# Kernel tuning notes

Measured on AMD Instinct MI355X. Metric: run time of the kernel, lower is better.

## Reference

```python
import math
import jax, jax.numpy as jnp
import numpy as np

B, T, E = 2, 2048, 1024
H, KV = 16, 4
D = E // H          # 64
G = H // KV         # 4 groups


def rotate_half(x):
    x1, x2 = jnp.split(x, 2, axis=-1)
    return jnp.concatenate([-x2, x1], axis=-1)


def setup_inputs() -> dict:
    key = jax.random.key(0)
    ks = jax.random.split(key, 12)
    query = jax.random.normal(ks[0], (B, T, E), jnp.float32)
    key_t = jax.random.normal(ks[1], (B, T, E), jnp.float32)
    value = jax.random.normal(ks[2], (B, T, E), jnp.float32)
    # RoPE tables: [T, D]
    inv_freq = 1.0 / (10000.0 ** (np.arange(0, D, 2, dtype=np.float32) / D))
    pos = np.arange(T, dtype=np.float32)
    freqs = np.outer(pos, inv_freq)                      # [T, D/2]
    emb = np.concatenate([freqs, freqs], axis=-1)        # [T, D]
    cos_emb = jnp.asarray(np.cos(emb), jnp.float32)
    sin_emb = jnp.asarray(np.sin(emb), jnp.float32)
    # causal mask [1,1,T,T], True = keep
    mask = jnp.tril(jnp.ones((T, T), bool))[None, None, :, :]
    s = 0.02
    Wq = jax.random.normal(ks[3], (E, H * D), jnp.float32) * s
    bq = jnp.zeros((H * D,), jnp.float32)
    Wk = jax.random.normal(ks[4], (E, KV * D), jnp.float32) * s
    bk = jnp.zeros((KV * D,), jnp.float32)
    Wv = jax.random.normal(ks[5], (E, KV * D), jnp.float32) * s
    bv = jnp.zeros((KV * D,), jnp.float32)
    Wo = jax.random.normal(ks[6], (E, E), jnp.float32) * s
    bo = jnp.zeros((E,), jnp.float32)
    return {"query": query, "key": key_t, "value": value,
            "cos_emb": cos_emb, "sin_emb": sin_emb, "mask": mask,
            "Wq": Wq, "bq": bq, "Wk": Wk, "bk": bk,
            "Wv": Wv, "bv": bv, "Wo": Wo, "bo": bo}


def reference(query, key, value, cos_emb, sin_emb, mask,
              Wq, bq, Wk, bk, Wv, bv, Wo, bo):
    Bq, Tq, _ = query.shape
    Tk = key.shape[1]
    q = (query @ Wq + bq).reshape(Bq, Tq, H, D)          # [B,Tq,H,D]
    k = (key @ Wk + bk).reshape(Bq, Tk, KV, D)           # [B,Tk,KV,D]
    v = (value @ Wv + bv).reshape(Bq, Tk, KV, D)
    # expand kv heads across groups (head h = kv*G + g, consecutive repeat)
    k = jnp.repeat(k, G, axis=2)                         # [B,Tk,H,D]
    v = jnp.repeat(v, G, axis=2)
    # RoPE (applied post-expansion, as in the original)
    cos = cos_emb[None, :, None, :]                      # [1,T,1,D]
    sin = sin_emb[None, :, None, :]
    q = q * cos[:, :Tq] + rotate_half(q) * sin[:, :Tq]
    k = k * cos[:, :Tk] + rotate_half(k) * sin[:, :Tk]
    scores = jnp.einsum('bqhd,bkhd->bhqk', q, k) / math.sqrt(D)
    scores = jnp.where(mask[:, :, :Tq, :Tk], scores, jnp.float32(-jnp.inf))
    probs = jax.nn.softmax(scores, axis=-1)              # [B,H,Tq,Tk]
    attn = jnp.einsum('bhqk,bkhd->bqhd', probs, v).reshape(Bq, Tq, E)
    return attn @ Wo + bo
```

## Files before the change

kernel.cpp:

```cpp
#include <hip/hip_runtime.h>
#include <hip/hip_bf16.h>

constexpr int Bc  = 2;
constexpr int Tc  = 2048;
constexpr int Ec  = 1024;
constexpr int Hc  = 16;
constexpr int KVc = 4;
constexpr int Dc  = 64;

typedef short bf16x8 __attribute__((ext_vector_type(8)));
typedef short short4v __attribute__((ext_vector_type(4)));
typedef float f32x4  __attribute__((ext_vector_type(4)));
typedef float f32x16 __attribute__((ext_vector_type(16)));
typedef int   i32x4  __attribute__((ext_vector_type(4)));

__device__ inline short f2bf_bits(float f) {
    union { __hip_bfloat16 h; short s; } u;
    u.h = __float2bfloat16(f);
    return u.s;
}

__device__ inline float bf2f(short s) {
    union { short s16; __hip_bfloat16 h; } u;
    u.s16 = s;
    return __bfloat162float(u.h);
}

__device__ inline unsigned pkbf(float a, float b) {
    union { __hip_bfloat162 h2; unsigned u; } u;
    u.h2 = __float22bfloat162_rn(float2{a, b});
    return u.u;
}

__device__ inline float fexp2(float x) { return __builtin_exp2f(x); }

__device__ inline void permswap(unsigned &a, unsigned &b) {
    asm volatile("v_permlane32_swap_b32 %0, %1" : "+v"(a), "+v"(b));
}

__device__ inline void gload16(const short* g, short* lds) {
    __builtin_amdgcn_global_load_lds(
        (const __attribute__((address_space(1))) unsigned int*)g,
        (__attribute__((address_space(3))) unsigned int*)lds,
        16, 0, 0);
}

__global__ __launch_bounds__(256) void transp_all(
    const float* __restrict__ Wq, const float* __restrict__ Wk,
    const float* __restrict__ Wv, const float* __restrict__ Wo,
    short* __restrict__ Wqt, short* __restrict__ Wkt,
    short* __restrict__ Wvt, short* __restrict__ Wot)
{
    __shared__ float tile[32][33];
    const int id = blockIdx.x;
    const float* W; short* Wt; int N, bx, by;
    if (id < 1024)      { W = Wq; Wt = Wqt; N = 1024; bx = id & 31;          by = id >> 5; }
    else if (id < 1280) { W = Wk; Wt = Wkt; N = 256;  bx = (id - 1024) & 7;  by = (id - 1024) >> 3; }
    else if (id < 1536) { W = Wv; Wt = Wvt; N = 256;  bx = (id - 1280) & 7;  by = (id - 1280) >> 3; }
    else                { W = Wo; Wt = Wot; N = 1024; bx = (id - 1536) & 31; by = (id - 1536) >> 5; }
    const int K = 1024;
    int nb = bx * 32, kb = by * 32;
    int tx = threadIdx.x & 31, ty = threadIdx.x >> 5;
    #pragma unroll
    for (int j = 0; j < 4; ++j)
        tile[ty + j * 8][tx] = W[(size_t)(kb + ty + j * 8) * N + nb + tx];
    __syncthreads();
    #pragma unroll
    for (int j = 0; j < 4; ++j)
        Wt[(size_t)(nb + ty + j * 8) * K + kb + tx] = f2bf_bits(tile[tx][ty + j * 8]);
}

__global__ __launch_bounds__(256) void gemm_qkv(
    const float* __restrict__ Xq, const float* __restrict__ Xk,
    const float* __restrict__ Xv,
    const short* __restrict__ Wqt, const short* __restrict__ Wkt,
    const short* __restrict__ Wvt,
    const float* __restrict__ bq, const float* __restrict__ bk,
    const float* __restrict__ bv,
    short* __restrict__ Qp, short* __restrict__ Kp, short* __restrict__ VTp)
{
    __shared__ short As[128 * 64];
    __shared__ short Bs[64 * 64];
    const int gid = blockIdx.x;
    const float* A; const short* Bt; const float* bias; int bx, by, mode;
    if (gid < 512)      { mode = 0; A = Xq; Bt = Wqt; bias = bq; bx = gid & 15;         by = gid >> 4; }
    else if (gid < 640) { mode = 1; A = Xk; Bt = Wkt; bias = bk; bx = (gid - 512) & 3;  by = (gid - 512) >> 2; }
    else                { mode = 2; A = Xv; Bt = Wvt; bias = bv; bx = (gid - 640) & 3;  by = (gid - 640) >> 2; }
    const int m0 = by * 128, n0 = bx * 64;

    const int lane = threadIdx.x & 63;
    const int w    = threadIdx.x >> 6;
    const int wm   = w >> 1, wn = w & 1;
    const int rin  = lane >> 3;
    const int swc  = ((lane & 7) ^ rin) * 8;

    f32x4 acc[4][2] = {};

    for (int k0 = 0; k0 < 1024; k0 += 64) {
        #pragma unroll
        for (int it = 0; it < 4; ++it) {
            int s   = threadIdx.x + it * 256;
            int row = s >> 3;
            int c8  = s & 7;
            const float* src = A + (size_t)(m0 + row) * 1024 + k0 + c8 * 8;
            float4 f0 = *reinterpret_cast<const float4*>(src);
            float4 f1 = *reinterpret_cast<const float4*>(src + 4);
            union { unsigned u4[4]; bf16x8 v; } pk;
            pk.u4[0] = pkbf(f0.x, f0.y);
            pk.u4[1] = pkbf(f0.z, f0.w);
            pk.u4[2] = pkbf(f1.x, f1.y);
            pk.u4[3] = pkbf(f1.z, f1.w);
            *reinterpret_cast<bf16x8*>(As + row * 64 + ((c8 ^ (row & 7)) * 8)) = pk.v;
        }
        #pragma unroll
        for (int i2 = 0; i2 < 2; ++i2) {
            const int r = w * 16 + i2 * 8;
            gload16(Bt + (size_t)(n0 + r + rin) * 1024 + k0 + swc, Bs + r * 64);
        }
        __syncthreads();
        #pragma unroll
        for (int ks = 0; ks < 2; ++ks) {
            bf16x8 af[4], bfr[2];
            #pragma unroll
            for (int mi = 0; mi < 4; ++mi) {
                int row = wm * 64 + mi * 16 + (lane & 15);
                int sl  = (ks * 4 + (lane >> 4)) ^ (row & 7);
                af[mi] = *reinterpret_cast<const bf16x8*>(As + row * 64 + sl * 8);
            }
            #pragma unroll
            for (int ni = 0; ni < 2; ++ni) {
                int row = wn * 32 + ni * 16 + (lane & 15);
                int sl  = (ks * 4 + (lane >> 4)) ^ (row & 7);
                bfr[ni] = *reinterpret_cast<const bf16x8*>(Bs + row * 64 + sl * 8);
            }
            #pragma unroll
            for (int mi = 0; mi < 4; ++mi)
                #pragma unroll
                for (int ni = 0; ni < 2; ++ni)
                    acc[mi][ni] = __builtin_amdgcn_mfma_f32_16x16x32_bf16(
                        af[mi], bfr[ni], acc[mi][ni], 0, 0, 0);
        }
        __syncthreads();
    }

    #pragma unroll
    for (int mi = 0; mi < 4; ++mi)
        #pragma unroll
        for (int ni = 0; ni < 2; ++ni) {
            int col = n0 + wn * 32 + ni * 16 + (lane & 15);
            float bv2 = bias[col];
            #pragma unroll
            for (int i = 0; i < 4; ++i) {
                int row = m0 + wm * 64 + mi * 16 + ((lane >> 4) * 4) + i;
                float v = acc[mi][ni][i] + bv2;
                if (mode == 0)
                    Qp[(size_t)row * 1024 + col] = f2bf_bits(v);
                else if (mode == 1)
                    Kp[(size_t)row * 256 + col] = f2bf_bits(v);
                else
                    VTp[(((size_t)(row >> 11) * 256 + col) << 11) + (row & 2047)]
                        = f2bf_bits(v);
            }
        }
}

__global__ __launch_bounds__(256) void gemm_o(
    const short* __restrict__ A, const short* __restrict__ Bt,
    const float* __restrict__ bias, float* __restrict__ C)
{
    __shared__ short As[128 * 64];
    __shared__ short Bs[64 * 64];
    const int m0 = blockIdx.y * 128, n0 = blockIdx.x * 64;

    const int lane = threadIdx.x & 63;
    const int w    = threadIdx.x >> 6;
    const int wm   = w >> 1, wn = w & 1;
    const int rin  = lane >> 3;
    const int swc  = ((lane & 7) ^ rin) * 8;

    f32x4 acc[4][2] = {};

    for (int k0 = 0; k0 < 1024; k0 += 64) {
        #pragma unroll
        for (int i2 = 0; i2 < 4; ++i2) {
            const int r = w * 32 + i2 * 8;
            gload16(A + (size_t)(m0 + r + rin) * 1024 + k0 + swc, As + r * 64);
        }
        #pragma unroll
        for (int i2 = 0; i2 < 2; ++i2) {
            const int r = w * 16 + i2 * 8;
            gload16(Bt + (size_t)(n0 + r + rin) * 1024 + k0 + swc, Bs + r * 64);
        }
        __syncthreads();
        #pragma unroll
        for (int ks = 0; ks < 2; ++ks) {
            bf16x8 af[4], bfr[2];
            #pragma unroll
            for (int mi = 0; mi < 4; ++mi) {
                int row = wm * 64 + mi * 16 + (lane & 15);
                int sl  = (ks * 4 + (lane >> 4)) ^ (row & 7);
                af[mi] = *reinterpret_cast<const bf16x8*>(As + row * 64 + sl * 8);
            }
            #pragma unroll
            for (int ni = 0; ni < 2; ++ni) {
                int row = wn * 32 + ni * 16 + (lane & 15);
                int sl  = (ks * 4 + (lane >> 4)) ^ (row & 7);
                bfr[ni] = *reinterpret_cast<const bf16x8*>(Bs + row * 64 + sl * 8);
            }
            #pragma unroll
            for (int mi = 0; mi < 4; ++mi)
                #pragma unroll
                for (int ni = 0; ni < 2; ++ni)
                    acc[mi][ni] = __builtin_amdgcn_mfma_f32_16x16x32_bf16(
                        af[mi], bfr[ni], acc[mi][ni], 0, 0, 0);
        }
        __syncthreads();
    }

    #pragma unroll
    for (int mi = 0; mi < 4; ++mi)
        #pragma unroll
        for (int ni = 0; ni < 2; ++ni) {
            int col = n0 + wn * 32 + ni * 16 + (lane & 15);
            float bv2 = bias[col];
            #pragma unroll
            for (int i = 0; i < 4; ++i) {
                int row = m0 + wm * 64 + mi * 16 + ((lane >> 4) * 4) + i;
                C[(size_t)row * 1024 + col] = acc[mi][ni][i] + bv2;
            }
        }
}

__global__ __launch_bounds__(256) void rope_k(
    short* __restrict__ Kp,
    const float* __restrict__ cosE, const float* __restrict__ sinE)
{
    int idx = blockIdx.x * 256 + threadIdx.x;
    int dq  = (idx & 7) * 4;
    int hh  = (idx >> 3) & 3;
    int row = idx >> 5;
    int t   = row & (Tc - 1);
    float4 c4 = *reinterpret_cast<const float4*>(cosE + t * 64 + dq);
    float4 s4 = *reinterpret_cast<const float4*>(sinE + t * 64 + dq);
    size_t base = (size_t)row * 256 + hh * 64 + dq;
    short4v a = *reinterpret_cast<const short4v*>(Kp + base);
    short4v b = *reinterpret_cast<const short4v*>(Kp + base + 32);
    short4v oa, ob;
    float c[4] = {c4.x, c4.y, c4.z, c4.w};
    float s[4] = {s4.x, s4.y, s4.z, s4.w};
    #pragma unroll
    for (int j = 0; j < 4; ++j) {
        float x1 = bf2f(a[j]), x2 = bf2f(b[j]);
        oa[j] = f2bf_bits(x1 * c[j] - x2 * s[j]);
        ob[j] = f2bf_bits(x2 * c[j] + x1 * s[j]);
    }
    *reinterpret_cast<short4v*>(Kp + base)      = oa;
    *reinterpret_cast<short4v*>(Kp + base + 32) = ob;
}

__global__ __launch_bounds__(256, 3) void flash_gqa9(
    const short* __restrict__ Q,
    const short* __restrict__ Kx,
    const short* __restrict__ VT,
    const float* __restrict__ cosE,
    const float* __restrict__ sinE,
    short* __restrict__ attn,
    short* __restrict__ PO,
    float* __restrict__ ML)
{
    __shared__ short smem[16384];

    const int lane = threadIdx.x & 63;
    const int w    = threadIdx.x >> 6;
    const int lo   = lane & 31;
    const int hi   = lane >> 5;

    const int L   = blockIdx.x;
    const int xcd = L & 7;
    const int j   = L >> 3;
    const int g   = j & 3;
    const int u   = 39 - (j >> 2);
    int qt = 0, rem = u;
    while (true) { int nc0 = (qt >> 2) + 1; if (rem < nc0) break; rem -= nc0; ++qt; }
    const int c  = rem;
    const int nc = (qt >> 2) + 1;
    const int b   = xcd >> 2;
    const int kvh = xcd & 3;
    const int h   = kvh * 4 + g;
    const int slot = (b * 16 + h) * 40 + u;

    const int q0w = qt * 128 + w * 32;
    const int qg  = q0w + lo;

    bf16x8 qf[4];
    {
        const short* qp = Q + (size_t)(b * Tc + qg) * Ec + h * 64 + hi * 8;
        const float* ct = cosE + (size_t)qg * 64 + hi * 8;
        const float* st = sinE + (size_t)qg * 64 + hi * 8;
        float qv[4][8], cv[4][8], sv[4][8];
        #pragma unroll
        for (int ds = 0; ds < 4; ++ds) {
            bf16x8 raw = *reinterpret_cast<const bf16x8*>(qp + 16 * ds);
            float4 c0 = *reinterpret_cast<const float4*>(ct + 16 * ds);
            float4 c1 = *reinterpret_cast<const float4*>(ct + 16 * ds + 4);
            float4 s0 = *reinterpret_cast<const float4*>(st + 16 * ds);
            float4 s1 = *reinterpret_cast<const float4*>(st + 16 * ds + 4);
            #pragma unroll
            for (int j2 = 0; j2 < 8; ++j2) qv[ds][j2] = bf2f(raw[j2]);
            cv[ds][0] = c0.x; cv[ds][1] = c0.y; cv[ds][2] = c0.z; cv[ds][3] = c0.w;
            cv[ds][4] = c1.x; cv[ds][5] = c1.y; cv[ds][6] = c1.z; cv[ds][7] = c1.w;
            sv[ds][0] = s0.x; sv[ds][1] = s0.y; sv[ds][2] = s0.z; sv[ds][3] = s0.w;
            sv[ds][4] = s1.x; sv[ds][5] = s1.y; sv[ds][6] = s1.z; sv[ds][7] = s1.w;
        }
        constexpr float SC = 0.125f * 1.44269504089f;
        #pragma unroll
        for (int ds = 0; ds < 2; ++ds) {
            #pragma unroll
            for (int j2 = 0; j2 < 8; j2 += 2) {
                float a0 = (qv[ds][j2]     * cv[ds][j2]     - qv[ds+2][j2]     * sv[ds][j2])     * SC;
                float a1 = (qv[ds][j2+1]   * cv[ds][j2+1]   - qv[ds+2][j2+1]   * sv[ds][j2+1])   * SC;
                float b0 = (qv[ds+2][j2]   * cv[ds+2][j2]   + qv[ds][j2]       * sv[ds+2][j2])   * SC;
                float b1 = (qv[ds+2][j2+1] * cv[ds+2][j2+1] + qv[ds][j2+1]     * sv[ds+2][j2+1]) * SC;
                reinterpret_cast<unsigned*>(&qf[ds])[j2 >> 1]     = pkbf(a0, a1);
                reinterpret_cast<unsigned*>(&qf[ds + 2])[j2 >> 1] = pkbf(b0, b1);
            }
        }
    }
    const short* Kb = Kx + (size_t)b * Tc * (KVc * Dc) + kvh * 64;
    const short* Vb = VT + (size_t)(b * KVc + kvh) * 64 * Tc;

    const int rin = lane >> 3;
    const int swc = ((lane & 7) ^ rin) * 8;
    auto stage = [&](int bufi, int kb2) {
        #pragma unroll
        for (int i2 = 0; i2 < 2; ++i2) {
            const int row = w * 16 + i2 * 8;
            gload16(Kb + (size_t)(kb2 + row + rin) * 256 + swc,
                    smem + bufi * 4096 + row * 64);
            gload16(Vb + (size_t)(row + rin) * Tc + kb2 + swc,
                    smem + 8192 + bufi * 4096 + row * 64);
        }
    };

    int slot8[4];
    #pragma unroll
    for (int i = 0; i < 4; ++i)
        slot8[i] = (((2 * i + hi) ^ (lo & 7)) * 8) + lo * 64;

    const int t0 = c * 8;
    const int t1 = min(c * 8 + 8, 2 * qt + 2);
    stage(0, t0 * 64);

    float m = -1e30f, l = 0.f;
    f32x16 o0 = {}, o1 = {};
    const int kv_hi = q0w + 32;

    for (int t = t0; t < t1; ++t) {
        const int kb  = t * 64;
        const int cur = (t - t0) & 1;
        asm volatile("s_waitcnt vmcnt(0)" ::: "memory");
        __builtin_amdgcn_s_barrier();
        if (t + 1 < t1) stage(cur ^ 1, kb + 64);

        if (kb < kv_hi) {
            const short* Kl = smem + cur * 4096;
            const short* Vl = Kl + 8192;

            bf16x8 kf0[4], kf1[4];
            #pragma unroll
            for (int ds = 0; ds < 4; ++ds) {
                kf0[ds] = *reinterpret_cast<const bf16x8*>(Kl + slot8[ds]);
                kf1[ds] = *reinterpret_cast<const bf16x8*>(Kl + slot8[ds] + 2048);
            }

            f32x16 s0 = {}, s1 = {};
            __builtin_amdgcn_s_setprio(1);
            #pragma unroll
            for (int ds = 0; ds < 4; ++ds) {
                s0 = __builtin_amdgcn_mfma_f32_32x32x16_bf16(kf0[ds], qf[ds], s0, 0, 0, 0);
                s1 = __builtin_amdgcn_mfma_f32_32x32x16_bf16(kf1[ds], qf[ds], s1, 0, 0, 0);
            }
            __builtin_amdgcn_s_setprio(0);

            bf16x8 vf0[4], vf1[4];
            #pragma unroll
            for (int sl = 0; sl < 4; ++sl) {
                vf0[sl] = *reinterpret_cast<const bf16x8*>(Vl + slot8[sl]);
                vf1[sl] = *reinterpret_cast<const bf16x8*>(Vl + slot8[sl] + 2048);
            }

            if (kb + 63 > q0w) {
                #pragma unroll
                for (int r = 0; r < 16; ++r) {
                    int kkl = (r & 3) + 8 * (r >> 2) + 4 * hi;
                    if (kb + kkl > qg)      s0[r] = -1e30f;
                    if (kb + 32 + kkl > qg) s1[r] = -1e30f;
                }
            }

            float mx[8];
            #pragma unroll
            for (int j2 = 0; j2 < 8; ++j2)
                mx[j2] = fmaxf(fmaxf(s0[2 * j2], s0[2 * j2 + 1]),
                               fmaxf(s1[2 * j2], s1[2 * j2 + 1]));
            #pragma unroll
            for (int st = 4; st > 0; st >>= 1)
                #pragma unroll
                for (int j2 = 0; j2 < st; ++j2) mx[j2] = fmaxf(mx[j2], mx[j2 + st]);
            float pm = fmaxf(mx[0], __shfl_xor(mx[0], 32));

            float corr = 1.0f;
            if (__any(pm > m + 8.0f)) {
                float mn = fmaxf(m, pm);
                corr = fexp2(m - mn);
                m = mn;
                #pragma unroll
                for (int r = 0; r < 16; ++r) { o0[r] *= corr; o1[r] *= corr; }
            }
            float rs = 0.f;
            #pragma unroll
            for (int r = 0; r < 16; ++r) {
                s0[r] = fexp2(s0[r] - m);
                s1[r] = fexp2(s1[r] - m);
                rs += s0[r] + s1[r];
            }
            rs += __shfl_xor(rs, 32);
            l = l * corr + rs;

            #pragma unroll
            for (int t2 = 0; t2 < 2; ++t2) {
                const f32x16& sv2 = t2 ? s1 : s0;
                unsigned pw[8];
                #pragma unroll
                for (int j2 = 0; j2 < 8; ++j2)
                    pw[j2] = pkbf(sv2[2 * j2], sv2[2 * j2 + 1]);
                #pragma unroll
                for (int u2 = 0; u2 < 2; ++u2) {
                    permswap(pw[4 * u2 + 0], pw[4 * u2 + 2]);
                    permswap(pw[4 * u2 + 1], pw[4 * u2 + 3]);
                    union { unsigned u4[4]; bf16x8 v; } pf;
                    pf.u4[0] = pw[4 * u2 + 0];
                    pf.u4[1] = pw[4 * u2 + 1];
                    pf.u4[2] = pw[4 * u2 + 2];
                    pf.u4[3] = pw[4 * u2 + 3];
                    int sl = 2 * t2 + u2;
                    __builtin_amdgcn_s_setprio(1);
                    o0 = __builtin_amdgcn_mfma_f32_32x32x16_bf16(vf0[sl], pf.v, o0, 0, 0, 0);
                    o1 = __builtin_amdgcn_mfma_f32_32x32x16_bf16(vf1[sl], pf.v, o1, 0, 0, 0);
                    __builtin_amdgcn_s_setprio(0);
                }
            }
        }
    }
    __builtin_amdgcn_s_barrier();

    const float inv = (nc == 1) ? (1.0f / l) : 1.0f;
    short* ob = smem + w * 2048;
    #pragma unroll
    for (int r = 0; r < 16; ++r) {
        int d0 = (r & 3) + 8 * (r >> 2) + 4 * hi;
        ob[lo * 64 + ( d0       ^ ((lo & 7) << 3))] = f2bf_bits(o0[r] * inv);
        ob[lo * 64 + ((d0 + 32) ^ ((lo & 7) << 3))] = f2bf_bits(o1[r] * inv);
    }
    if (nc > 1 && hi == 0) {
        ML[(size_t)slot * 256 + (w * 32 + lo) * 2]     = m;
        ML[(size_t)slot * 256 + (w * 32 + lo) * 2 + 1] = l;
    }
    #pragma unroll
    for (int j2 = 0; j2 < 4; ++j2) {
        int row = lane >> 1;
        int c8  = ((lane & 1) * 4 + j2) * 8;
        bf16x8 v = *reinterpret_cast<const bf16x8*>(
            ob + row * 64 + (c8 ^ ((row & 7) << 3)));
        if (nc == 1)
            *reinterpret_cast<bf16x8*>(
                attn + (size_t)(b * Tc + q0w + row) * Ec + h * 64 + c8) = v;
        else
            *reinterpret_cast<bf16x8*>(
                PO + (size_t)slot * 8192 + (w * 32 + row) * 64 + c8) = v;
    }
}

__global__ __launch_bounds__(256) void combine_kernel(
    const short* __restrict__ PO, const float* __restrict__ ML,
    short* __restrict__ attn)
{
    const int qt    = 4 + (blockIdx.x >> 2);
    const int rg    = blockIdx.x & 3;
    const int combo = blockIdx.y;
    const int h = combo & 15, b = combo >> 4;
    const int nc = (qt >> 2) + 1;
    const int k  = qt >> 2, r4 = qt & 3;
    const int base = (k + 1) * (2 * k + r4);
    const int slot0 = combo * 40 + base;

    const int r  = rg * 32 + (threadIdx.x >> 3);
    const int d8 = (threadIdx.x & 7) * 8;

    float mv[4], lv[4];
    float M = -1e30f;
    #pragma unroll 4
    for (int cc = 0; cc < nc; ++cc) {
        mv[cc] = ML[(size_t)(slot0 + cc) * 256 + r * 2];
        lv[cc] = ML[(size_t)(slot0 + cc) * 256 + r * 2 + 1];
        M = fmaxf(M, mv[cc]);
    }
    float Lsum = 0.f;
    float a[8] = {};
    #pragma unroll 4
    for (int cc = 0; cc < nc; ++cc) {
        float wgt = fexp2(mv[cc] - M);
        Lsum += wgt * lv[cc];
        bf16x8 po = *reinterpret_cast<const bf16x8*>(
            PO + (size_t)(slot0 + cc) * 8192 + r * 64 + d8);
        #pragma unroll
        for (int j = 0; j < 8; ++j) a[j] += wgt * bf2f(po[j]);
    }
    float inv = 1.0f / Lsum;
    bf16x8 o;
    #pragma unroll
    for (int j = 0; j < 8; ++j) o[j] = f2bf_bits(a[j] * inv);
    *reinterpret_cast<bf16x8*>(
        attn + (size_t)(b * Tc + qt * 128 + r) * Ec + h * 64 + d8) = o;
}

extern "C" void kernel_launch(void* const* d_in, const int* in_sizes, int n_in,
                              void* d_out, int out_size, void* d_ws, size_t ws_size,
                              hipStream_t stream)
{
    const float* query = (const float*)d_in[0];
    const float* key   = (const float*)d_in[1];
    const float* value = (const float*)d_in[2];
    const float* cosE  = (const float*)d_in[3];
    const float* sinE  = (const float*)d_in[4];
    const float* Wq = (const float*)d_in[6];
    const float* bq = (const float*)d_in[7];
    const float* Wk = (const float*)d_in[8];
    const float* bk = (const float*)d_in[9];
    const float* Wv = (const float*)d_in[10];
    const float* bv = (const float*)d_in[11];
    const float* Wo = (const float*)d_in[12];
    const float* bo = (const float*)d_in[13];

    char* ws = (char*)d_ws;
    constexpr size_t MB = 1u << 20;
    short* PO   = (short*)(ws + 0);
    float* ML   = (float*)(ws + 21 * MB);
    short* Wqt  = (short*)(ws + 24 * MB);
    short* Wkt  = (short*)(ws + 26 * MB);
    short* Wvt  = (short*)(ws + 26 * MB + 512 * 1024);
    short* Wot  = (short*)(ws + 27 * MB);
    short* Qp   = (short*)(ws + 29 * MB);
    short* Kp   = (short*)(ws + 37 * MB);
    short* VTp  = (short*)(ws + 39 * MB);
    short* attn = (short*)(ws + 41 * MB);
    (void)ws_size;

    transp_all<<<2560, 256, 0, stream>>>(Wq, Wk, Wv, Wo, Wqt, Wkt, Wvt, Wot);
    gemm_qkv<<<768, 256, 0, stream>>>(query, key, value, Wqt, Wkt, Wvt,
                                      bq, bk, bv, Qp, Kp, VTp);
    rope_k<<<512, 256, 0, stream>>>(Kp, cosE, sinE);
    flash_gqa9<<<1280, 256, 0, stream>>>(Qp, Kp, VTp, cosE, sinE, attn, PO, ML);
    combine_kernel<<<dim3(48, 32), 256, 0, stream>>>(PO, ML, attn);
    gemm_o<<<dim3(16, 32), 256, 0, stream>>>(attn, Wot, bo, (float*)d_out);
}
```

Measured before the change: 133.4 us.

## Fuse RoPE into QKV GEMM epilogue, pre-convert query to bf16, lighten flash registers

Adds a kernel that converts the query activations to bf16 so the Q-projection GEMM can stream its A tile into shared memory through global_load_lds. Q and K RoPE, together with the softmax scale for Q, now run in the GEMM epilogue via a shared-memory staged tile, which removes the separate rope_k kernel and the per-block Q RoPE in the flash kernel. The flash kernel loads K and V fragments just before each MFMA rather than holding them all in registers, and its launch bound rises from 3 to 4 waves per SIMD to raise occupancy. In exchange it adds an extra pass over the query input and one more kernel launch.

```diff
diff --git a/kernel.cpp b/kernel.cpp
--- a/kernel.cpp
+++ b/kernel.cpp
@@ -43,6 +43,19 @@
         (const __attribute__((address_space(1))) unsigned int*)g,
         (__attribute__((address_space(3))) unsigned int*)lds,
         16, 0, 0);
+}
+
+__global__ __launch_bounds__(256) void conv_q(
+    const float* __restrict__ q, short* __restrict__ Xq)
+{
+    int i = (blockIdx.x * 256 + threadIdx.x) * 4;
+    float4 vv = *reinterpret_cast<const float4*>(q + i);
+    short4v o;
+    o[0] = f2bf_bits(vv.x);
+    o[1] = f2bf_bits(vv.y);
+    o[2] = f2bf_bits(vv.z);
+    o[3] = f2bf_bits(vv.w);
+    *reinterpret_cast<short4v*>(Xq + i) = o;
 }
 
 __global__ __launch_bounds__(256) void transp_all(
@@ -71,21 +84,23 @@
 }
 
 __global__ __launch_bounds__(256) void gemm_qkv(
-    const float* __restrict__ Xq, const float* __restrict__ Xk,
-    const float* __restrict__ Xv,
+    const short* __restrict__ Xq,
+    const float* __restrict__ keyF, const float* __restrict__ valF,
     const short* __restrict__ Wqt, const short* __restrict__ Wkt,
     const short* __restrict__ Wvt,
     const float* __restrict__ bq, const float* __restrict__ bk,
     const float* __restrict__ bv,
+    const float* __restrict__ cosE, const float* __restrict__ sinE,
     short* __restrict__ Qp, short* __restrict__ Kp, short* __restrict__ VTp)
 {
     __shared__ short As[128 * 64];
     __shared__ short Bs[64 * 64];
     const int gid = blockIdx.x;
-    const float* A; const short* Bt; const float* bias; int bx, by, mode;
-    if (gid < 512)      { mode = 0; A = Xq; Bt = Wqt; bias = bq; bx = gid & 15;         by = gid >> 4; }
-    else if (gid < 640) { mode = 1; A = Xk; Bt = Wkt; bias = bk; bx = (gid - 512) & 3;  by = (gid - 512) >> 2; }
-    else                { mode = 2; A = Xv; Bt = Wvt; bias = bv; bx = (gid - 640) & 3;  by = (gid - 640) >> 2; }
+    const short* Bt; const float* bias; int bx, by, mode;
+    const float* Af = nullptr;
+    if (gid < 512)      { mode = 0; Bt = Wqt; bias = bq; bx = gid & 15;        by = gid >> 4; }
+    else if (gid < 640) { mode = 1; Af = keyF; Bt = Wkt; bias = bk; bx = (gid - 512) & 3; by = (gid - 512) >> 2; }
+    else                { mode = 2; Af = valF; Bt = Wvt; bias = bv; bx = (gid - 640) & 3; by = (gid - 640) >> 2; }
     const int m0 = by * 128, n0 = bx * 64;
 
     const int lane = threadIdx.x & 63;
@@ -97,20 +112,28 @@
     f32x4 acc[4][2] = {};
 
     for (int k0 = 0; k0 < 1024; k0 += 64) {
-        #pragma unroll
-        for (int it = 0; it < 4; ++it) {
-            int s   = threadIdx.x + it * 256;
-            int row = s >> 3;
-            int c8  = s & 7;
-            const float* src = A + (size_t)(m0 + row) * 1024 + k0 + c8 * 8;
-            float4 f0 = *reinterpret_cast<const float4*>(src);
-            float4 f1 = *reinterpret_cast<const float4*>(src + 4);
-            union { unsigned u4[4]; bf16x8 v; } pk;
-            pk.u4[0] = pkbf(f0.x, f0.y);
-            pk.u4[1] = pkbf(f0.z, f0.w);
-            pk.u4[2] = pkbf(f1.x, f1.y);
-            pk.u4[3] = pkbf(f1.z, f1.w);
-            *reinterpret_cast<bf16x8*>(As + row * 64 + ((c8 ^ (row & 7)) * 8)) = pk.v;
+        if (mode == 0) {
+            #pragma unroll
+            for (int i2 = 0; i2 < 4; ++i2) {
+                const int r = w * 32 + i2 * 8;
+                gload16(Xq + (size_t)(m0 + r + rin) * 1024 + k0 + swc, As + r * 64);
+            }
+        } else {
+            #pragma unroll
+            for (int it = 0; it < 4; ++it) {
+                int s   = threadIdx.x + it * 256;
+                int row = s >> 3;
+                int c8  = s & 7;
+                const float* src = Af + (size_t)(m0 + row) * 1024 + k0 + c8 * 8;
+                float4 f0 = *reinterpret_cast<const float4*>(src);
+                float4 f1 = *reinterpret_cast<const float4*>(src + 4);
+                union { unsigned u4[4]; bf16x8 v; } pk;
+                pk.u4[0] = pkbf(f0.x, f0.y);
+                pk.u4[1] = pkbf(f0.z, f0.w);
+                pk.u4[2] = pkbf(f1.x, f1.y);
+                pk.u4[3] = pkbf(f1.z, f1.w);
+                *reinterpret_cast<bf16x8*>(As + row * 64 + ((c8 ^ (row & 7)) * 8)) = pk.v;
+            }
         }
         #pragma unroll
         for (int i2 = 0; i2 < 2; ++i2) {
@@ -143,25 +166,63 @@
         __syncthreads();
     }
 
+    if (mode == 2) {
+        #pragma unroll
+        for (int mi = 0; mi < 4; ++mi)
+            #pragma unroll
+            for (int ni = 0; ni < 2; ++ni) {
+                int col = n0 + wn * 32 + ni * 16 + (lane & 15);
+                float bv2 = bias[col];
+                #pragma unroll
+                for (int i = 0; i < 4; ++i) {
+                    int row = m0 + wm * 64 + mi * 16 + ((lane >> 4) * 4) + i;
+                    VTp[(((size_t)(row >> 11) * 256 + col) << 11) + (row & 2047)]
+                        = f2bf_bits(acc[mi][ni][i] + bv2);
+                }
+            }
+        return;
+    }
+
     #pragma unroll
     for (int mi = 0; mi < 4; ++mi)
         #pragma unroll
         for (int ni = 0; ni < 2; ++ni) {
-            int col = n0 + wn * 32 + ni * 16 + (lane & 15);
-            float bv2 = bias[col];
+            int cl = wn * 32 + ni * 16 + (lane & 15);
+            float bv2 = bias[n0 + cl];
             #pragma unroll
             for (int i = 0; i < 4; ++i) {
-                int row = m0 + wm * 64 + mi * 16 + ((lane >> 4) * 4) + i;
-                float v = acc[mi][ni][i] + bv2;
-                if (mode == 0)
-                    Qp[(size_t)row * 1024 + col] = f2bf_bits(v);
-                else if (mode == 1)
-                    Kp[(size_t)row * 256 + col] = f2bf_bits(v);
-                else
-                    VTp[(((size_t)(row >> 11) * 256 + col) << 11) + (row & 2047)]
-                        = f2bf_bits(v);
-            }
-        }
+                int rl = wm * 64 + mi * 16 + ((lane >> 4) * 4) + i;
+                As[rl * 64 + cl] = f2bf_bits(acc[mi][ni][i] + bv2);
+            }
+        }
+    __syncthreads();
+
+    const float scale = (mode == 0) ? 0.125f * 1.44269504089f : 1.0f;
+    short* outp = (mode == 0) ? Qp : Kp;
+    const int ldo = (mode == 0) ? 1024 : 256;
+    const int dg  = (threadIdx.x & 7) * 4;
+    const int rb  = threadIdx.x >> 3;
+    #pragma unroll
+    for (int rr = 0; rr < 4; ++rr) {
+        int rl = rb + rr * 32;
+        int t  = (m0 + rl) & (Tc - 1);
+        float4 c4 = *reinterpret_cast<const float4*>(cosE + t * 64 + dg);
+        float4 s4 = *reinterpret_cast<const float4*>(sinE + t * 64 + dg);
+        short4v a = *reinterpret_cast<const short4v*>(As + rl * 64 + dg);
+        short4v b = *reinterpret_cast<const short4v*>(As + rl * 64 + 32 + dg);
+        float c[4] = {c4.x, c4.y, c4.z, c4.w};
+        float s[4] = {s4.x, s4.y, s4.z, s4.w};
+        short4v oa, ob;
+        #pragma unroll
+        for (int j = 0; j < 4; ++j) {
+            float x1 = bf2f(a[j]), x2 = bf2f(b[j]);
+            oa[j] = f2bf_bits((x1 * c[j] - x2 * s[j]) * scale);
+            ob[j] = f2bf_bits((x2 * c[j] + x1 * s[j]) * scale);
+        }
+        size_t go = (size_t)(m0 + rl) * ldo + n0 + dg;
+        *reinterpret_cast<short4v*>(outp + go)      = oa;
+        *reinterpret_cast<short4v*>(outp + go + 32) = ob;
+    }
 }
 
 __global__ __launch_bounds__(256) void gemm_o(
@@ -231,39 +292,10 @@
         }
 }
 
-__global__ __launch_bounds__(256) void rope_k(
-    short* __restrict__ Kp,
-    const float* __restrict__ cosE, const float* __restrict__ sinE)
-{
-    int idx = blockIdx.x * 256 + threadIdx.x;
-    int dq  = (idx & 7) * 4;
-    int hh  = (idx >> 3) & 3;
-    int row = idx >> 5;
-    int t   = row & (Tc - 1);
-    float4 c4 = *reinterpret_cast<const float4*>(cosE + t * 64 + dq);
-    float4 s4 = *reinterpret_cast<const float4*>(sinE + t * 64 + dq);
-    size_t base = (size_t)row * 256 + hh * 64 + dq;
-    short4v a = *reinterpret_cast<const short4v*>(Kp + base);
-    short4v b = *reinterpret_cast<const short4v*>(Kp + base + 32);
-    short4v oa, ob;
-    float c[4] = {c4.x, c4.y, c4.z, c4.w};
-    float s[4] = {s4.x, s4.y, s4.z, s4.w};
-    #pragma unroll
-    for (int j = 0; j < 4; ++j) {
-        float x1 = bf2f(a[j]), x2 = bf2f(b[j]);
-        oa[j] = f2bf_bits(x1 * c[j] - x2 * s[j]);
-        ob[j] = f2bf_bits(x2 * c[j] + x1 * s[j]);
-    }
-    *reinterpret_cast<short4v*>(Kp + base)      = oa;
-    *reinterpret_cast<short4v*>(Kp + base + 32) = ob;
-}
-
-__global__ __launch_bounds__(256, 3) void flash_gqa9(
+__global__ __launch_bounds__(256, 4) void flash_gqa10(
     const short* __restrict__ Q,
     const short* __restrict__ Kx,
     const short* __restrict__ VT,
-    const float* __restrict__ cosE,
-    const float* __restrict__ sinE,
     short* __restrict__ attn,
     short* __restrict__ PO,
     float* __restrict__ ML)
@@ -295,36 +327,9 @@
     bf16x8 qf[4];
     {
         const short* qp = Q + (size_t)(b * Tc + qg) * Ec + h * 64 + hi * 8;
-        const float* ct = cosE + (size_t)qg * 64 + hi * 8;
-        const float* st = sinE + (size_t)qg * 64 + hi * 8;
-        float qv[4][8], cv[4][8], sv[4][8];
-        #pragma unroll
-        for (int ds = 0; ds < 4; ++ds) {
-            bf16x8 raw = *reinterpret_cast<const bf16x8*>(qp + 16 * ds);
-            float4 c0 = *reinterpret_cast<const float4*>(ct + 16 * ds);
-            float4 c1 = *reinterpret_cast<const float4*>(ct + 16 * ds + 4);
-            float4 s0 = *reinterpret_cast<const float4*>(st + 16 * ds);
-            float4 s1 = *reinterpret_cast<const float4*>(st + 16 * ds + 4);
-            #pragma unroll
-            for (int j2 = 0; j2 < 8; ++j2) qv[ds][j2] = bf2f(raw[j2]);
-            cv[ds][0] = c0.x; cv[ds][1] = c0.y; cv[ds][2] = c0.z; cv[ds][3] = c0.w;
-            cv[ds][4] = c1.x; cv[ds][5] = c1.y; cv[ds][6] = c1.z; cv[ds][7] = c1.w;
-            sv[ds][0] = s0.x; sv[ds][1] = s0.y; sv[ds][2] = s0.z; sv[ds][3] = s0.w;
-            sv[ds][4] = s1.x; sv[ds][5] = s1.y; sv[ds][6] = s1.z; sv[ds][7] = s1.w;
-        }
-        constexpr float SC = 0.125f * 1.44269504089f;
-        #pragma unroll
-        for (int ds = 0; ds < 2; ++ds) {
-            #pragma unroll
-            for (int j2 = 0; j2 < 8; j2 += 2) {
-                float a0 = (qv[ds][j2]     * cv[ds][j2]     - qv[ds+2][j2]     * sv[ds][j2])     * SC;
-                float a1 = (qv[ds][j2+1]   * cv[ds][j2+1]   - qv[ds+2][j2+1]   * sv[ds][j2+1])   * SC;
-                float b0 = (qv[ds+2][j2]   * cv[ds+2][j2]   + qv[ds][j2]       * sv[ds+2][j2])   * SC;
-                float b1 = (qv[ds+2][j2+1] * cv[ds+2][j2+1] + qv[ds][j2+1]     * sv[ds+2][j2+1]) * SC;
-                reinterpret_cast<unsigned*>(&qf[ds])[j2 >> 1]     = pkbf(a0, a1);
-                reinterpret_cast<unsigned*>(&qf[ds + 2])[j2 >> 1] = pkbf(b0, b1);
-            }
-        }
+        #pragma unroll
+        for (int ds = 0; ds < 4; ++ds)
+            qf[ds] = *reinterpret_cast<const bf16x8*>(qp + 16 * ds);
     }
     const short* Kb = Kx + (size_t)b * Tc * (KVc * Dc) + kvh * 64;
     const short* Vb = VT + (size_t)(b * KVc + kvh) * 64 * Tc;
@@ -366,28 +371,16 @@
             const short* Kl = smem + cur * 4096;
             const short* Vl = Kl + 8192;
 
-            bf16x8 kf0[4], kf1[4];
-            #pragma unroll
-            for (int ds = 0; ds < 4; ++ds) {
-                kf0[ds] = *reinterpret_cast<const bf16x8*>(Kl + slot8[ds]);
-                kf1[ds] = *reinterpret_cast<const bf16x8*>(Kl + slot8[ds] + 2048);
-            }
-
             f32x16 s0 = {}, s1 = {};
             __builtin_amdgcn_s_setprio(1);
             #pragma unroll
             for (int ds = 0; ds < 4; ++ds) {
-                s0 = __builtin_amdgcn_mfma_f32_32x32x16_bf16(kf0[ds], qf[ds], s0, 0, 0, 0);
-                s1 = __builtin_amdgcn_mfma_f32_32x32x16_bf16(kf1[ds], qf[ds], s1, 0, 0, 0);
+                bf16x8 k0 = *reinterpret_cast<const bf16x8*>(Kl + slot8[ds]);
+                bf16x8 k1 = *reinterpret_cast<const bf16x8*>(Kl + slot8[ds] + 2048);
+                s0 = __builtin_amdgcn_mfma_f32_32x32x16_bf16(k0, qf[ds], s0, 0, 0, 0);
+                s1 = __builtin_amdgcn_mfma_f32_32x32x16_bf16(k1, qf[ds], s1, 0, 0, 0);
             }
             __builtin_amdgcn_s_setprio(0);
-
-            bf16x8 vf0[4], vf1[4];
-            #pragma unroll
-            for (int sl = 0; sl < 4; ++sl) {
-                vf0[sl] = *reinterpret_cast<const bf16x8*>(Vl + slot8[sl]);
-                vf1[sl] = *reinterpret_cast<const bf16x8*>(Vl + slot8[sl] + 2048);
-            }
 
             if (kb + 63 > q0w) {
                 #pragma unroll
@@ -429,11 +422,11 @@
 
             #pragma unroll
             for (int t2 = 0; t2 < 2; ++t2) {
-                const f32x16& sv2 = t2 ? s1 : s0;
+                const f32x16& sv = t2 ? s1 : s0;
                 unsigned pw[8];
                 #pragma unroll
                 for (int j2 = 0; j2 < 8; ++j2)
-                    pw[j2] = pkbf(sv2[2 * j2], sv2[2 * j2 + 1]);
+                    pw[j2] = pkbf(sv[2 * j2], sv[2 * j2 + 1]);
                 #pragma unroll
                 for (int u2 = 0; u2 < 2; ++u2) {
                     permswap(pw[4 * u2 + 0], pw[4 * u2 + 2]);
@@ -444,9 +437,11 @@
                     pf.u4[2] = pw[4 * u2 + 2];
                     pf.u4[3] = pw[4 * u2 + 3];
                     int sl = 2 * t2 + u2;
+                    bf16x8 v0 = *reinterpret_cast<const bf16x8*>(Vl + slot8[sl]);
+                    bf16x8 v1 = *reinterpret_cast<const bf16x8*>(Vl + slot8[sl] + 2048);
                     __builtin_amdgcn_s_setprio(1);
-                    o0 = __builtin_amdgcn_mfma_f32_32x32x16_bf16(vf0[sl], pf.v, o0, 0, 0, 0);
-                    o1 = __builtin_amdgcn_mfma_f32_32x32x16_bf16(vf1[sl], pf.v, o1, 0, 0, 0);
+                    o0 = __builtin_amdgcn_mfma_f32_32x32x16_bf16(v0, pf.v, o0, 0, 0, 0);
+                    o1 = __builtin_amdgcn_mfma_f32_32x32x16_bf16(v1, pf.v, o1, 0, 0, 0);
                     __builtin_amdgcn_s_setprio(0);
                 }
             }
@@ -544,8 +539,7 @@
 
     char* ws = (char*)d_ws;
     constexpr size_t MB = 1u << 20;
-    short* PO   = (short*)(ws + 0);
-    float* ML   = (float*)(ws + 21 * MB);
+    short* Xq   = (short*)(ws + 0);
     short* Wqt  = (short*)(ws + 24 * MB);
     short* Wkt  = (short*)(ws + 26 * MB);
     short* Wvt  = (short*)(ws + 26 * MB + 512 * 1024);
@@ -554,13 +548,15 @@
     short* Kp   = (short*)(ws + 37 * MB);
     short* VTp  = (short*)(ws + 39 * MB);
     short* attn = (short*)(ws + 41 * MB);
+    short* PO   = (short*)(ws + 0);
+    float* ML   = (float*)(ws + 21 * MB);
     (void)ws_size;
 
+    conv_q<<<4096, 256, 0, stream>>>(query, Xq);
     transp_all<<<2560, 256, 0, stream>>>(Wq, Wk, Wv, Wo, Wqt, Wkt, Wvt, Wot);
-    gemm_qkv<<<768, 256, 0, stream>>>(query, key, value, Wqt, Wkt, Wvt,
-                                      bq, bk, bv, Qp, Kp, VTp);
-    rope_k<<<512, 256, 0, stream>>>(Kp, cosE, sinE);
-    flash_gqa9<<<1280, 256, 0, stream>>>(Qp, Kp, VTp, cosE, sinE, attn, PO, ML);
+    gemm_qkv<<<768, 256, 0, stream>>>(Xq, key, value, Wqt, Wkt, Wvt,
+                                      bq, bk, bv, cosE, sinE, Qp, Kp, VTp);
+    flash_gqa10<<<1280, 256, 0, stream>>>(Qp, Kp, VTp, attn, PO, ML);
     combine_kernel<<<dim3(48, 32), 256, 0, stream>>>(PO, ML, attn);
     gemm_o<<<dim3(16, 32), 256, 0, stream>>>(attn, Wot, bo, (float*)d_out);
 }
```

Result: faster. 116.6 us (-12.6%).
